# Kernel optimization log

Measured on AMD Instinct MI355X. Metric: run time of the kernel, lower is better.

## Reference

```python
import jax, jax.numpy as jnp
import numpy as np

SLOPE = 0.01  # LeakyReLU default negative slope
EPS = 1e-5    # BatchNorm eps


def _lrelu(x):
    return jnp.where(x >= 0, x, SLOPE * x)


def _conv(x, w, b):
    # x: [B,C,H,W], w: [O,I,kh,kw] (torch layout)
    y = jax.lax.conv_general_dilated(x, w, (1, 1), 'VALID',
                                     dimension_numbers=('NCHW', 'OIHW', 'NCHW'))
    return y + b[None, :, None, None]


def _bn4(x, p):
    # eval-mode BatchNorm2d; p = [gamma, beta, running_mean, running_var] stacked [4,C]
    g, b, m, v = p
    s = g * jax.lax.rsqrt(v + EPS)
    return x * s[None, :, None, None] + (b - m * s)[None, :, None, None]


def _forward(observation, action, sc1_w, sc1_b, sbn1, sc2_w, sc2_b, sbn2,
             mc1_w, mc1_b, mbn1, mc2_w, mc2_b, mbn2,
             gw_root, gw_rel, g_b, gbn,
             a_cw, a_cb, a_w1, a_b1, a_w2, a_b2, a_w3, a_b3,
             edge_index, edge_type, nodes_to_select):
    # ---- multi-scale temporal CNN (eval mode: dropout = identity) ----
    s = _lrelu(_bn4(_conv(observation, sc1_w, sc1_b), sbn1))
    s = _lrelu(_bn4(_conv(s, sc2_w, sc2_b), sbn2))          # [B,20,N,1]
    m = _lrelu(_bn4(_conv(observation, mc1_w, mc1_b), mbn1))
    m = _lrelu(_bn4(_conv(m, mc2_w, mc2_b), mbn2))          # [B,20,N,1]
    l = _lrelu(jnp.max(observation, axis=3, keepdims=True)) # [B,3,N,1]
    temporal = jnp.concatenate([s, m, l], axis=1)           # [B,43,N,1]

    # ---- RGCN (graph replicated per batch element; aggr='mean' per relation) ----
    x = jnp.swapaxes(temporal[..., 0], 1, 2)                # [B,N,F]
    N = x.shape[1]
    src, dst = edge_index[0], edge_index[1]
    out = jnp.einsum('bnf,fg->bng', x, gw_root) + g_b       # root transform + bias
    for r in range(gw_rel.shape[0]):
        h = jnp.einsum('bnf,fg->bng', x, gw_rel[r])         # per-relation transform
        mask = (edge_type == r).astype(x.dtype)             # [E]
        msgs = h[:, src, :] * mask[None, :, None]           # [B,E,F] gather
        agg = jax.ops.segment_sum(jnp.swapaxes(msgs, 0, 1), dst, num_segments=N)  # [N,B,F]
        deg = jax.ops.segment_sum(mask, dst, num_segments=N)                       # [N]
        out = out + jnp.swapaxes(agg, 0, 1) / jnp.maximum(deg, 1.0)[None, :, None]
    # BatchNorm1d (eval) + LeakyReLU; dropout = identity
    g, be, mu, v = gbn
    sg = g * jax.lax.rsqrt(v + EPS)
    out = _lrelu(out * sg + (be - mu * sg))                 # [B,N,F]

    graph_feats = jnp.swapaxes(out, 1, 2)[..., None]        # [B,F,N,1]
    feats = jnp.concatenate([temporal, graph_feats], axis=1)  # [B,86,N,1]
    feats = feats[:, :, nodes_to_select, :]                 # [B,86,P,1]

    # ---- actor head (mode == 'actor'); cash_bias is zeroed in the original ----
    stocks = action[:, 1:][:, None, :, None]                # [B,1,P,1]
    f = jnp.concatenate([stocks, feats], axis=1)[..., 0]    # [B,87,P]
    logits = jnp.einsum('bcp,c->bp', f, a_cw) + a_cb[0]     # 1x1 conv, out_ch=1
    o = jnp.concatenate([jnp.zeros((f.shape[0], 1), f.dtype), logits], axis=1)  # [B,P+1]
    h1 = jax.nn.relu(o @ a_w1 + a_b1)
    h2 = jax.nn.relu(h1 @ a_w2 + a_b2)
    return jax.nn.softmax(h2 @ a_w3 + a_b3, axis=-1)


def setup_inputs() -> dict:
    key = jax.random.key(0)
    ks = jax.random.split(key, 30)
    B, C0, N, T = 64, 3, 500, 50
    E, R, P, H = 16000, 4, 500, 128
    CM, CF = 3, 20
    F = 2 * CF + C0  # 43

    def rn(k, sh, s=0.1):
        return jax.random.normal(k, sh, jnp.float32) * s

    def bn_p(k, c):
        k1, k2, k3, k4 = jax.random.split(k, 4)
        return jnp.stack([jax.random.uniform(k1, (c,), jnp.float32, 0.5, 1.5),
                          rn(k2, (c,)), rn(k3, (c,)),
                          jax.random.uniform(k4, (c,), jnp.float32, 0.5, 1.5)])

    return {
        'observation': jax.random.normal(ks[0], (B, C0, N, T), jnp.float32),
        'action': jax.random.uniform(ks[1], (B, P + 1), jnp.float32),
        'edge_index': jax.random.randint(ks[2], (2, E), 0, N),
        'edge_type': jax.random.randint(ks[3], (E,), 0, R),
        'nodes_to_select': jnp.arange(P),
        'sc1_w': rn(ks[4], (CM, C0, 1, 3)), 'sc1_b': rn(ks[5], (CM,)), 'sbn1': bn_p(ks[6], CM),
        'sc2_w': rn(ks[7], (CF, CM, 1, 48)), 'sc2_b': rn(ks[8], (CF,)), 'sbn2': bn_p(ks[9], CF),
        'mc1_w': rn(ks[10], (CM, C0, 1, 21)), 'mc1_b': rn(ks[11], (CM,)), 'mbn1': bn_p(ks[12], CM),
        'mc2_w': rn(ks[13], (CF, CM, 1, 30)), 'mc2_b': rn(ks[14], (CF,)), 'mbn2': bn_p(ks[15], CF),
        'gw_root': rn(ks[16], (F, F)), 'gw_rel': rn(ks[17], (R, F, F)),
        'g_b': rn(ks[18], (F,)), 'gbn': bn_p(ks[19], F),
        'a_cw': rn(ks[20], (2 * F + 1,)), 'a_cb': rn(ks[21], (1,)),
        'a_w1': rn(ks[22], (P + 1, H)), 'a_b1': rn(ks[23], (H,)),
        'a_w2': rn(ks[24], (H, H)), 'a_b2': rn(ks[25], (H,)),
        'a_w3': rn(ks[26], (H, P + 1)), 'a_b3': rn(ks[27], (P + 1,)),
    }


def reference(observation, action, edge_index, edge_type, nodes_to_select,
              sc1_w, sc1_b, sbn1, sc2_w, sc2_b, sbn2,
              mc1_w, mc1_b, mbn1, mc2_w, mc2_b, mbn2,
              gw_root, gw_rel, g_b, gbn,
              a_cw, a_cb, a_w1, a_b1, a_w2, a_b2, a_w3, a_b3):
    return _forward(observation, action, sc1_w, sc1_b, sbn1, sc2_w, sc2_b, sbn2,
                    mc1_w, mc1_b, mbn1, mc2_w, mc2_b, mbn2,
                    gw_root, gw_rel, g_b, gbn,
                    a_cw, a_cb, a_w1, a_b1, a_w2, a_b2, a_w3, a_b3,
                    edge_index, edge_type, nodes_to_select)
```

## Files before the change

kernel.cpp:

```cpp
#include <hip/hip_runtime.h>

#define SLOPE 0.01f
#define EPSV  1e-5f
#define BB    64
#define NN    500
#define TT    50
#define E_N   16000
#define FF    43
#define PP    500
#define HH    128
#define XSTRIDE 48
#define PAD_E 40

typedef const float* fp;

__device__ __forceinline__ float lrelu(float x){ return x >= 0.f ? x : SLOPE * x; }
__device__ __forceinline__ float bnap(float x, fp bnp, int c, int C){
  float g  = bnp[c], b_ = bnp[C + c];
  float m  = bnp[2*C + c], v = bnp[3*C + c];
  float s = g * rsqrtf(v + EPSV);
  return x * s + (b_ - m * s);
}

#define DPP_I(x, c) __builtin_amdgcn_update_dpp(0, (x), (c), 0xF, 0xF, true)
__device__ __forceinline__ float rsum16(float x){
  x += __int_as_float(DPP_I(__float_as_int(x), 0xB1));
  x += __int_as_float(DPP_I(__float_as_int(x), 0x4E));
  x += __int_as_float(DPP_I(__float_as_int(x), 0x124));
  x += __int_as_float(DPP_I(__float_as_int(x), 0x128));
  return x;
}
__device__ __forceinline__ float rmax16(float x){
  x = fmaxf(x, __int_as_float(DPP_I(__float_as_int(x), 0xB1)));
  x = fmaxf(x, __int_as_float(DPP_I(__float_as_int(x), 0x4E)));
  x = fmaxf(x, __int_as_float(DPP_I(__float_as_int(x), 0x124)));
  x = fmaxf(x, __int_as_float(DPP_I(__float_as_int(x), 0x128)));
  return x;
}

__global__ __launch_bounds__(512) void k_tempo24(
    fp obs, fp sc1w, fp mc1w, fp sc2w, fp mc2w,
    fp sc1b, fp sbn1, fp sc2b, fp sbn2,
    fp mc1b, fp mbn1, fp mc2b, fp mbn2,
    const int* __restrict__ ei, const int* __restrict__ et,
    int* __restrict__ cntg, int* __restrict__ esp,
    float* __restrict__ xbuf)
{
  __shared__ float OL[4896];
  __shared__ float WSr[2880];
  __shared__ float WMr[1800];
  __shared__ float TBL[100];
  int tid  = threadIdx.x;
  int w    = tid >> 6, lane = tid & 63;
  int node = lane >> 4, seg = lane & 15;
  int gg   = __builtin_amdgcn_readfirstlane(blockIdx.x*8 + w);
  int b    = gg / 125, ng = gg - b*125;
  int n0   = ng * 4;
  int wbase = w * 612;

  for (int i = tid; i < 720; i += 512) *(float4*)(WSr + i*4) = *(const float4*)(sc2w + i*4);
  for (int i = tid; i < 450; i += 512) *(float4*)(WMr + i*4) = *(const float4*)(mc2w + i*4);

  if (tid < 20){
    float g = sbn2[tid], b_ = sbn2[20+tid], m = sbn2[40+tid], v = sbn2[60+tid];
    float s = g * rsqrtf(v + EPSV);
    TBL[tid] = s; TBL[43+tid] = sc2b[tid]*s + (b_ - m*s);
  } else if (tid < 40){
    int o = tid - 20;
    float g = mbn2[o], b_ = mbn2[20+o], m = mbn2[40+o], v = mbn2[60+o];
    float s = g * rsqrtf(v + EPSV);
    TBL[tid] = s; TBL[43+tid] = mc2b[o]*s + (b_ - m*s);
  } else if (tid < 43){
    TBL[tid] = 1.f; TBL[43+tid] = 0.f;
  } else if (tid < 46){
    int ci = tid - 43;
    float g = sbn1[ci], b_ = sbn1[3+ci], m = sbn1[6+ci], v = sbn1[9+ci];
    float s = g * rsqrtf(v + EPSV);
    TBL[86+ci] = s; TBL[89+ci] = sc1b[ci]*s + (b_ - m*s);
  } else if (tid < 49){
    int ci = tid - 46;
    float g = mbn1[ci], b_ = mbn1[3+ci], m = mbn1[6+ci], v = mbn1[9+ci];
    float s = g * rsqrtf(v + EPSV);
    TBL[92+ci] = s; TBL[95+ci] = mc1b[ci]*s + (b_ - m*s);
  }

  if (blockIdx.x < 8){
    int base = blockIdx.x * 2000;
    #pragma unroll
    for (int k = 0; k < 4; k++){
      int el = k*512 + tid;
      if (el < 2000){
        int e = base + el;
        int s = ei[e], d = ei[E_N + e], r = et[e];
        int idx = d*4 + r;
        int pos = atomicAdd(&cntg[idx], 1);
        if (pos < PAD_E) esp[idx*PAD_E + pos] = s;
      }
    }
  }

  for (int c = 0; c < 3; c++){
    if (lane < 50){
      const float4 v = *(const float4*)(obs + ((size_t)(b*3+c)*NN + n0)*TT + lane*4);
      int f = lane*4;
      int n = f/50, t = f - n*50;
      int a = wbase + c*204 + n*51 + t;
      OL[a] = v.x;
      if (++t == 50){ t = 0; n++; a = wbase + c*204 + n*51; } else a++;
      OL[a] = v.y;
      if (++t == 50){ t = 0; n++; a = wbase + c*204 + n*51; } else a++;
      OL[a] = v.z;
      if (++t == 50){ t = 0; n++; a = wbase + c*204 + n*51; } else a++;
      OL[a] = v.w;
    }
  }
  __syncthreads();

  int rb = wbase + node*51;
  int g  = b*NN + n0 + node;
  float* xr = xbuf + (size_t)g * XSTRIDE;
  float acc[20];

  {
    float mv[3][3];
    #pragma unroll
    for (int i = 0; i < 3; i++)
      #pragma unroll
      for (int co = 0; co < 3; co++) mv[i][co] = 0.f;
    int t0 = seg*3;
    #pragma unroll
    for (int ci = 0; ci < 3; ci++){
      int ab = rb + ci*204 + t0;
      float v0 = OL[ab], v1 = OL[ab+1], v2 = OL[ab+2], v3 = OL[ab+3], v4 = OL[ab+4];
      #pragma unroll
      for (int co = 0; co < 3; co++){
        float w0 = sc1w[co*9+ci*3+0], w1 = sc1w[co*9+ci*3+1], w2 = sc1w[co*9+ci*3+2];
        mv[0][co] += v0*w0 + v1*w1 + v2*w2;
        mv[1][co] += v1*w0 + v2*w1 + v3*w2;
        mv[2][co] += v2*w0 + v3*w1 + v4*w2;
      }
    }
    #pragma unroll
    for (int o = 0; o < 20; o++) acc[o] = 0.f;
    #pragma unroll
    for (int i = 0; i < 3; i++){
      int tt = t0 + i;
      #pragma unroll
      for (int co = 0; co < 3; co++){
        float z = lrelu(mv[i][co]*TBL[86+co] + TBL[89+co]);
        const float* wr = WSr + co*48 + tt;
        #pragma unroll
        for (int o = 0; o < 20; o++)
          acc[o] += z * wr[o*144];
      }
    }
    #pragma unroll
    for (int o = 0; o < 20; o++) acc[o] = rsum16(acc[o]);
    #pragma unroll
    for (int o = 0; o < 20; o++)
      if (seg == (o & 15)) xr[o] = lrelu(acc[o]*TBL[o] + TBL[43+o]);
  }

  {
    float mv[2][3];
    #pragma unroll
    for (int i = 0; i < 2; i++)
      #pragma unroll
      for (int co = 0; co < 3; co++) mv[i][co] = 0.f;
    int t0 = seg*2;
    #pragma unroll
    for (int ci = 0; ci < 3; ci++){
      int ab = rb + ci*204 + t0;
      float vc = OL[ab];
      #pragma unroll
      for (int k = 0; k < 21; k++){
        float vn = OL[ab + k + 1];
        #pragma unroll
        for (int co = 0; co < 3; co++){
          float wk = mc1w[co*63 + ci*21 + k];
          mv[0][co] += vc*wk;
          mv[1][co] += vn*wk;
        }
        vc = vn;
      }
    }
    #pragma unroll
    for (int o = 0; o < 20; o++) acc[o] = 0.f;
    if (seg < 15){
      #pragma unroll
      for (int co = 0; co < 3; co++){
        float z0 = lrelu(mv[0][co]*TBL[92+co] + TBL[95+co]);
        float z1 = lrelu(mv[1][co]*TBL[92+co] + TBL[95+co]);
        const float* wr = WMr + co*30 + t0;
        #pragma unroll
        for (int o = 0; o < 20; o++){
          float2 q = *(const float2*)(wr + o*90);
          acc[o] += z0*q.x + z1*q.y;
        }
      }
    }
    #pragma unroll
    for (int o = 0; o < 20; o++) acc[o] = rsum16(acc[o]);
    #pragma unroll
    for (int o = 0; o < 20; o++)
      if (seg == (o & 15)) xr[20+o] = lrelu(acc[o]*TBL[20+o] + TBL[63+o]);
  }

  {
    float m0 = -3e38f, m1 = -3e38f, m2 = -3e38f;
    int l0 = seg*4;
    int ln = 50 - l0; if (ln > 4) ln = 4;
    for (int j = 0; j < ln; j++){
      m0 = fmaxf(m0, OL[rb +       l0 + j]);
      m1 = fmaxf(m1, OL[rb + 204 + l0 + j]);
      m2 = fmaxf(m2, OL[rb + 408 + l0 + j]);
    }
    m0 = rmax16(m0); m1 = rmax16(m1); m2 = rmax16(m2);
    if (seg == 0) xr[40] = lrelu(m0);
    if (seg == 1) xr[41] = lrelu(m1);
    if (seg == 2) xr[42] = lrelu(m2);
  }
}

__global__ __launch_bounds__(1024) void k_graph20(
    const float* __restrict__ xbuf,
    fp gwroot, fp gwrel, fp gb, fp gbnp,
    const int* __restrict__ cntg, const int* __restrict__ esp,
    fp action, fp acw, fp acb,
    float* __restrict__ o_ws)
{
  __shared__ float xin[64][219];
  __shared__ float lred[16][64];
  int n = blockIdx.x;
  int tid = threadIdx.x;
  int w = tid >> 6, lane = tid & 63;
  int b0 = w * 4;

  const float* xb0 = xbuf + (size_t)((b0+0)*NN) * XSTRIDE;
  const float* xb1 = xbuf + (size_t)((b0+1)*NN) * XSTRIDE;
  const float* xb2 = xbuf + (size_t)((b0+2)*NN) * XSTRIDE;
  const float* xb3 = xbuf + (size_t)((b0+3)*NN) * XSTRIDE;

  if (lane < FF){
    xin[b0+0][lane] = xb0[(size_t)n*XSTRIDE + lane];
    xin[b0+1][lane] = xb1[(size_t)n*XSTRIDE + lane];
    xin[b0+2][lane] = xb2[(size_t)n*XSTRIDE + lane];
    xin[b0+3][lane] = xb3[(size_t)n*XSTRIDE + lane];
  }

  #pragma unroll
  for (int r = 0; r < 4; r++){
    int idx = n*4 + r;
    int c = __builtin_amdgcn_readfirstlane(cntg[idx]);
    if (c > PAD_E) c = PAD_E;
    const int* ep = esp + idx*PAD_E;
    float a0 = 0.f, a1 = 0.f, a2 = 0.f, a3 = 0.f;
    int i = 0;
    for (; i + 4 <= c; i += 4){
      int s0 = ep[i], s1 = ep[i+1], s2 = ep[i+2], s3 = ep[i+3];
      size_t o0 = (size_t)s0*XSTRIDE + lane, o1 = (size_t)s1*XSTRIDE + lane;
      size_t o2 = (size_t)s2*XSTRIDE + lane, o3 = (size_t)s3*XSTRIDE + lane;
      if (lane < FF){
        a0 += xb0[o0] + xb0[o1] + xb0[o2] + xb0[o3];
        a1 += xb1[o0] + xb1[o1] + xb1[o2] + xb1[o3];
        a2 += xb2[o0] + xb2[o1] + xb2[o2] + xb2[o3];
        a3 += xb3[o0] + xb3[o1] + xb3[o2] + xb3[o3];
      }
    }
    for (; i < c; i++){
      int s = ep[i];
      size_t o = (size_t)s*XSTRIDE + lane;
      if (lane < FF){
        a0 += xb0[o]; a1 += xb1[o]; a2 += xb2[o]; a3 += xb3[o];
      }
    }
    float inv = 1.f / fmaxf((float)c, 1.f);
    if (lane < FF){
      xin[b0+0][43 + 43*r + lane] = a0 * inv;
      xin[b0+1][43 + 43*r + lane] = a1 * inv;
      xin[b0+2][43 + 43*r + lane] = a2 * inv;
      xin[b0+3][43 + 43*r + lane] = a3 * inv;
    }
  }
  __syncthreads();

  int c0 = __builtin_amdgcn_readfirstlane(w * 3);
  float acc[3];
  #pragma unroll
  for (int j = 0; j < 3; j++) acc[j] = (c0 + j < FF) ? gb[c0+j] : 0.f;
  for (int f = 0; f < 43; f++){
    float v = xin[lane][f];
    const float* wp = gwroot + f*43 + c0;
    #pragma unroll
    for (int j = 0; j < 3; j++) acc[j] += v * wp[j];
  }
  for (int f = 0; f < 172; f++){
    float v = xin[lane][43 + f];
    const float* wp = gwrel + f*43 + c0;
    #pragma unroll
    for (int j = 0; j < 3; j++) acc[j] += v * wp[j];
  }
  float lp = 0.f;
  #pragma unroll
  for (int j = 0; j < 3; j++){
    int c = c0 + j;
    if (c < FF){
      float gv = lrelu(bnap(acc[j], gbnp, c, FF));
      lp += gv * acw[1 + FF + c];
    }
  }
  if (w == 15){
    float xp = acb[0] + action[lane*(PP+1) + 1 + n] * acw[0];
    #pragma unroll 2
    for (int c = 0; c < FF; c++) xp += xin[lane][c] * acw[1 + c];
    lp = xp;
  }
  lred[w][lane] = lp;
  __syncthreads();
  if (tid < 64){
    float t = 0.f;
    #pragma unroll
    for (int w2 = 0; w2 < 16; w2++) t += lred[w2][tid];
    o_ws[tid*(PP+1) + 1 + n] = t;
  }
}

__global__ __launch_bounds__(512) void k_fcall2(
    const float* __restrict__ o_ws,
    fp aw1, fp ab1, fp aw2, fp ab2, fp aw3, fp ab3,
    float* __restrict__ out)
{
  int b = blockIdx.x;
  int tid = threadIdx.x;
  __shared__ float os[PP+1];
  __shared__ float part[4][HH];
  __shared__ float h1[HH];
  __shared__ float h2[HH];
  __shared__ float red[512];

  if (tid <= PP) os[tid] = (tid == 0) ? 0.f : o_ws[b*(PP+1) + tid];
  __syncthreads();

  {
    int chunk = tid >> 7, h = tid & 127;
    int k0 = chunk * 125;
    int kn = (chunk == 3) ? 126 : 125;
    float acc = 0.f;
    for (int k = 0; k < kn; k++) acc += os[k0+k] * aw1[(k0+k)*HH + h];
    part[chunk][h] = acc;
  }
  __syncthreads();
  if (tid < HH)
    h1[tid] = fmaxf(ab1[tid] + part[0][tid] + part[1][tid] + part[2][tid] + part[3][tid], 0.f);
  __syncthreads();
  if (tid < HH){
    float acc = ab2[tid];
    #pragma unroll 4
    for (int k = 0; k < HH; k++) acc += h1[k] * aw2[k*HH + tid];
    h2[tid] = fmaxf(acc, 0.f);
  }
  __syncthreads();

  float val = -1e30f;
  if (tid <= PP){
    float acc = ab3[tid];
    #pragma unroll 4
    for (int k = 0; k < HH; k++) acc += h2[k] * aw3[k*(PP+1) + tid];
    val = acc;
  }
  red[tid] = val;
  __syncthreads();
  for (int s = 256; s > 0; s >>= 1){
    if (tid < s) red[tid] = fmaxf(red[tid], red[tid + s]);
    __syncthreads();
  }
  float mxv = red[0];
  __syncthreads();
  float e = (tid <= PP) ? expf(val - mxv) : 0.f;
  red[tid] = e;
  __syncthreads();
  for (int s = 256; s > 0; s >>= 1){
    if (tid < s) red[tid] += red[tid + s];
    __syncthreads();
  }
  float sum = red[0];
  if (tid <= PP) out[b*(PP+1) + tid] = e / sum;
}

extern "C" void kernel_launch(void* const* d_in, const int* in_sizes, int n_in,
                              void* d_out, int out_size, void* d_ws, size_t ws_size,
                              hipStream_t stream)
{
  fp obs    = (fp)d_in[0];
  fp action = (fp)d_in[1];
  const int* ei  = (const int*)d_in[2];
  const int* et  = (const int*)d_in[3];
  fp sc1w=(fp)d_in[5],  sc1b=(fp)d_in[6],  sbn1=(fp)d_in[7];
  fp sc2w=(fp)d_in[8],  sc2b=(fp)d_in[9],  sbn2=(fp)d_in[10];
  fp mc1w=(fp)d_in[11], mc1b=(fp)d_in[12], mbn1=(fp)d_in[13];
  fp mc2w=(fp)d_in[14], mc2b=(fp)d_in[15], mbn2=(fp)d_in[16];
  fp gwroot=(fp)d_in[17], gwrel=(fp)d_in[18], gb=(fp)d_in[19], gbnp=(fp)d_in[20];
  fp acw=(fp)d_in[21], acb=(fp)d_in[22];
  fp aw1=(fp)d_in[23], ab1=(fp)d_in[24];
  fp aw2=(fp)d_in[25], ab2=(fp)d_in[26];
  fp aw3=(fp)d_in[27], ab3=(fp)d_in[28];

  float* xbuf   = (float*)d_ws;
  float* o_ws   = xbuf + 1536000;
  int*   cntg   = (int*)(o_ws + 32064);
  int*   esp    = cntg + 2000;

  float* out = (float*)d_out;

  hipMemsetAsync(cntg, 0, 2000*sizeof(int), stream);
  hipLaunchKernelGGL(k_tempo24, dim3(1000), dim3(512), 0, stream,
    obs, sc1w, mc1w, sc2w, mc2w,
    sc1b, sbn1, sc2b, sbn2, mc1b, mbn1, mc2b, mbn2,
    ei, et, cntg, esp, xbuf);
  hipLaunchKernelGGL(k_graph20, dim3(500), dim3(1024), 0, stream,
    xbuf, gwroot, gwrel, gb, gbnp, cntg, esp, action, acw, acb, o_ws);
  hipLaunchKernelGGL(k_fcall2, dim3(BB), dim3(512), 0, stream,
    o_ws, aw1, ab1, aw2, ab2, aw3, ab3, out);
}
```

Measured before the change: 216.8 us.

## Build per-node edge lists in shared memory inside graph kernel, drop memset

Removes the global edge-bucketing pass (atomics into a global count/list buffer) from the temporal kernel, along with the memset that cleared it. Each graph block instead scans all 16000 edges, keeps those whose destination is its node, and builds per-relation source lists in shared memory with shared atomics. This saves a memset call and the global atomics, but every one of the 500 blocks now reads the full edge arrays, which is far more total (mostly cached) traffic and adds a block-wide sync.

```diff
diff --git a/kernel.cpp b/kernel.cpp
--- a/kernel.cpp
+++ b/kernel.cpp
@@ -38,12 +38,10 @@
   return x;
 }
 
-__global__ __launch_bounds__(512) void k_tempo24(
+__global__ __launch_bounds__(512) void k_tempo26(
     fp obs, fp sc1w, fp mc1w, fp sc2w, fp mc2w,
     fp sc1b, fp sbn1, fp sc2b, fp sbn2,
     fp mc1b, fp mbn1, fp mc2b, fp mbn2,
-    const int* __restrict__ ei, const int* __restrict__ et,
-    int* __restrict__ cntg, int* __restrict__ esp,
     float* __restrict__ xbuf)
 {
   __shared__ float OL[4896];
@@ -84,21 +82,6 @@
     TBL[92+ci] = s; TBL[95+ci] = mc1b[ci]*s + (b_ - m*s);
   }
 
-  if (blockIdx.x < 8){
-    int base = blockIdx.x * 2000;
-    #pragma unroll
-    for (int k = 0; k < 4; k++){
-      int el = k*512 + tid;
-      if (el < 2000){
-        int e = base + el;
-        int s = ei[e], d = ei[E_N + e], r = et[e];
-        int idx = d*4 + r;
-        int pos = atomicAdd(&cntg[idx], 1);
-        if (pos < PAD_E) esp[idx*PAD_E + pos] = s;
-      }
-    }
-  }
-
   for (int c = 0; c < 3; c++){
     if (lane < 50){
       const float4 v = *(const float4*)(obs + ((size_t)(b*3+c)*NN + n0)*TT + lane*4);
@@ -222,15 +205,17 @@
   }
 }
 
-__global__ __launch_bounds__(1024) void k_graph20(
+__global__ __launch_bounds__(1024) void k_graph21(
     const float* __restrict__ xbuf,
+    const int* __restrict__ ei, const int* __restrict__ et,
     fp gwroot, fp gwrel, fp gb, fp gbnp,
-    const int* __restrict__ cntg, const int* __restrict__ esp,
     fp action, fp acw, fp acb,
     float* __restrict__ o_ws)
 {
   __shared__ float xin[64][219];
   __shared__ float lred[16][64];
+  __shared__ int cnt[4];
+  __shared__ int lst[4][PAD_E];
   int n = blockIdx.x;
   int tid = threadIdx.x;
   int w = tid >> 6, lane = tid & 63;
@@ -240,6 +225,18 @@
   const float* xb1 = xbuf + (size_t)((b0+1)*NN) * XSTRIDE;
   const float* xb2 = xbuf + (size_t)((b0+2)*NN) * XSTRIDE;
   const float* xb3 = xbuf + (size_t)((b0+3)*NN) * XSTRIDE;
+
+  if (tid < 4) cnt[tid] = 0;
+  __syncthreads();
+
+  for (int e = tid; e < E_N; e += 1024){
+    int d = ei[E_N + e];
+    if (d == n){
+      int r = et[e];
+      int pos = atomicAdd(&cnt[r], 1);
+      if (pos < PAD_E) lst[r][pos] = ei[e];
+    }
+  }
 
   if (lane < FF){
     xin[b0+0][lane] = xb0[(size_t)n*XSTRIDE + lane];
@@ -247,17 +244,16 @@
     xin[b0+2][lane] = xb2[(size_t)n*XSTRIDE + lane];
     xin[b0+3][lane] = xb3[(size_t)n*XSTRIDE + lane];
   }
+  __syncthreads();
 
   #pragma unroll
   for (int r = 0; r < 4; r++){
-    int idx = n*4 + r;
-    int c = __builtin_amdgcn_readfirstlane(cntg[idx]);
+    int c = cnt[r];
     if (c > PAD_E) c = PAD_E;
-    const int* ep = esp + idx*PAD_E;
     float a0 = 0.f, a1 = 0.f, a2 = 0.f, a3 = 0.f;
     int i = 0;
     for (; i + 4 <= c; i += 4){
-      int s0 = ep[i], s1 = ep[i+1], s2 = ep[i+2], s3 = ep[i+3];
+      int s0 = lst[r][i], s1 = lst[r][i+1], s2 = lst[r][i+2], s3 = lst[r][i+3];
       size_t o0 = (size_t)s0*XSTRIDE + lane, o1 = (size_t)s1*XSTRIDE + lane;
       size_t o2 = (size_t)s2*XSTRIDE + lane, o3 = (size_t)s3*XSTRIDE + lane;
       if (lane < FF){
@@ -268,7 +264,7 @@
       }
     }
     for (; i < c; i++){
-      int s = ep[i];
+      int s = lst[r][i];
       size_t o = (size_t)s*XSTRIDE + lane;
       if (lane < FF){
         a0 += xb0[o]; a1 += xb1[o]; a2 += xb2[o]; a3 += xb3[o];
@@ -407,18 +403,15 @@
 
   float* xbuf   = (float*)d_ws;
   float* o_ws   = xbuf + 1536000;
-  int*   cntg   = (int*)(o_ws + 32064);
-  int*   esp    = cntg + 2000;
 
   float* out = (float*)d_out;
 
-  hipMemsetAsync(cntg, 0, 2000*sizeof(int), stream);
-  hipLaunchKernelGGL(k_tempo24, dim3(1000), dim3(512), 0, stream,
+  hipLaunchKernelGGL(k_tempo26, dim3(1000), dim3(512), 0, stream,
     obs, sc1w, mc1w, sc2w, mc2w,
     sc1b, sbn1, sc2b, sbn2, mc1b, mbn1, mc2b, mbn2,
-    ei, et, cntg, esp, xbuf);
-  hipLaunchKernelGGL(k_graph20, dim3(500), dim3(1024), 0, stream,
-    xbuf, gwroot, gwrel, gb, gbnp, cntg, esp, action, acw, acb, o_ws);
+    xbuf);
+  hipLaunchKernelGGL(k_graph21, dim3(500), dim3(1024), 0, stream,
+    xbuf, ei, et, gwroot, gwrel, gb, gbnp, action, acw, acb, o_ws);
   hipLaunchKernelGGL(k_fcall2, dim3(BB), dim3(512), 0, stream,
     o_ws, aw1, ab1, aw2, ab2, aw3, ab3, out);
 }
```

After: 215.6 us. Within noise of the previous version (-0.6%).
